# Kernel tuning notes

Measured on AMD Instinct MI355X. Metric: run time of the kernel, lower is better.

## Reference

```python
import jax, jax.numpy as jnp
import numpy as np

D = 1024
H = 16

def setup_inputs() -> dict:
    key = jax.random.key(0)
    k1, k2, k3 = jax.random.split(key, 3)
    x = jax.random.normal(k1, (2, 2048, D), dtype=jnp.float32)
    # torch Linear weights: qkv (3d, d), proj (d, d); y = x @ W.T
    w_qkv = jax.random.normal(k2, (3 * D, D), dtype=jnp.float32) * (1.0 / np.sqrt(D))
    w_proj = jax.random.normal(k3, (D, D), dtype=jnp.float32) * (1.0 / np.sqrt(D))
    return {"x": x, "w_qkv": w_qkv, "w_proj": w_proj}

def reference(x, w_qkv, w_proj):
    B, T, C = x.shape
    hd = C // H  # head dim
    qkv = x @ w_qkv.T                     # [B,T,3C]
    q, k, v = jnp.split(qkv, 3, axis=-1)
    q = q.reshape(B, T, H, hd).transpose(0, 2, 1, 3)  # [B,H,T,hd]
    k = k.reshape(B, T, H, hd).transpose(0, 2, 1, 3)
    v = v.reshape(B, T, H, hd).transpose(0, 2, 1, 3)
    att = jnp.einsum('bhqd,bhkd->bhqk', q, k) * (hd ** -0.5)  # [B,H,T,T]
    mask = jnp.triu(jnp.ones((T, T), dtype=bool), 1)
    att = jnp.where(mask, jnp.float32(-1e9), att)
    att = jax.nn.softmax(att, axis=-1)
    y = jnp.einsum('bhqk,bhkd->bhqd', att, v)  # [B,H,T,hd]
    y = y.transpose(0, 2, 1, 3).reshape(B, T, C)
    return y @ w_proj.T
```

## Files before the change

kernel.cpp:

```cpp
#include <hip/hip_runtime.h>
#include <hip/hip_bf16.h>


typedef __bf16 bf16;
typedef __bf16 bf16x8 __attribute__((ext_vector_type(8)));
typedef float f32x4 __attribute__((ext_vector_type(4)));

__device__ __forceinline__ bf16 f2bf(float f) {
    unsigned u = __builtin_bit_cast(unsigned, f);
    u += 0x7fffu + ((u >> 16) & 1u);
    unsigned short h = (unsigned short)(u >> 16);
    return __builtin_bit_cast(bf16, h);
}
__device__ __forceinline__ bf16 trunc_bf(float f) {
    unsigned u = __builtin_bit_cast(unsigned, f);
    return __builtin_bit_cast(bf16, (unsigned short)(u >> 16));
}

__device__ __forceinline__ bf16x8 ld8f(const float* p) {
    f32x4 a = *(const f32x4*)p;
    f32x4 b = *(const f32x4*)(p + 4);
    bf16x8 r;
#pragma unroll
    for (int i = 0; i < 4; i++) { r[i] = f2bf(a[i]); r[i + 4] = f2bf(b[i]); }
    return r;
}

__device__ __forceinline__ void st_out(bf16* p, float v)  { *p = f2bf(v); }
__device__ __forceinline__ void st_out(float* p, float v) { *p = v; }

__global__ __launch_bounds__(256) void cvt_bf16(const float* __restrict__ src,
                                                bf16* __restrict__ dst, int n) {
    int i = (blockIdx.x * 256 + threadIdx.x) * 8;
    if (i < n) *(bf16x8*)&dst[i] = ld8f(&src[i]);
}

__device__ __forceinline__ void glds16(const bf16* g, bf16* l) {
    __builtin_amdgcn_global_load_lds(
        (const __attribute__((address_space(1))) void*)g,
        (__attribute__((address_space(3))) void*)l, 16, 0, 0);
}

template <typename TC, int BN>
__global__ __launch_bounds__(256) void gemm_glds(const bf16* __restrict__ A, int lda, int aoff,
                                                 const bf16* __restrict__ W,
                                                 TC* __restrict__ C, int N, int K) {
    constexpr int NI = (BN == 128) ? 4 : 2;
    __shared__ bf16 sA[128 * 32];
    __shared__ bf16 sW[BN * 32];
    const int bm = blockIdx.x * 128, bn = blockIdx.y * BN;
    const int tid = threadIdx.x;
    const int wave = tid >> 6, lane = tid & 63;
    const int quad = lane >> 4, l16 = lane & 15;
    const int rbase = (BN == 128) ? (wave >> 1) * 64 : wave * 32;
    const int cbase = (BN == 128) ? (wave & 1) * 64 : 0;
    const int r16 = lane >> 2, cl = lane & 3;
    const int gch = cl ^ ((r16 >> 1) & 3);
    const int sl  = (l16 >> 1) & 3;

    f32x4 acc[NI][4] = {};

    for (int k0 = 0; k0 < K; k0 += 32) {
        __syncthreads();
#pragma unroll
        for (int t = 0; t < 2; t++) {
            int row = wave * 32 + t * 16 + r16;
            glds16(&A[(size_t)(bm + row) * lda + aoff + k0 + gch * 8],
                   &sA[(wave * 32 + t * 16) * 32]);
        }
        if (BN == 128) {
#pragma unroll
            for (int t = 0; t < 2; t++) {
                int row = wave * 32 + t * 16 + r16;
                glds16(&W[(size_t)(bn + row) * K + k0 + gch * 8],
                       &sW[(wave * 32 + t * 16) * 32]);
            }
        } else {
            int row = wave * 16 + r16;
            glds16(&W[(size_t)(bn + row) * K + k0 + gch * 8], &sW[(wave * 16) * 32]);
        }
        __syncthreads();

        bf16x8 af[NI], bfr[4];
#pragma unroll
        for (int i = 0; i < NI; i++)
            af[i] = *(bf16x8*)&sA[(rbase + i * 16 + l16) * 32 + (quad ^ sl) * 8];
#pragma unroll
        for (int j = 0; j < 4; j++)
            bfr[j] = *(bf16x8*)&sW[(cbase + j * 16 + l16) * 32 + (quad ^ sl) * 8];
#pragma unroll
        for (int i = 0; i < NI; i++)
#pragma unroll
            for (int j = 0; j < 4; j++)
                acc[i][j] = __builtin_amdgcn_mfma_f32_16x16x32_bf16(
                    af[i], bfr[j], acc[i][j], 0, 0, 0);
    }

#pragma unroll
    for (int i = 0; i < NI; i++)
#pragma unroll
        for (int j = 0; j < 4; j++)
#pragma unroll
            for (int r = 0; r < 4; r++) {
                int row = bm + rbase + i * 16 + quad * 4 + r;
                int col = bn + cbase + j * 16 + l16;
                st_out(&C[(size_t)row * N + col], acc[i][j][r]);
            }
}

__global__ __launch_bounds__(256) void transpose_v(const bf16* __restrict__ qkv,
                                                   bf16* __restrict__ vt) {
    __shared__ bf16 s[64][72];
    const int tt = blockIdx.x;
    const int bh = blockIdx.y;
    const int b = bh >> 4, h = bh & 15;
    const int tid = threadIdx.x;

    for (int c = tid; c < 512; c += 256) {
        int t = c >> 3, dc = (c & 7) * 8;
        *(bf16x8*)&s[t][dc] =
            *(const bf16x8*)&qkv[((size_t)(b * 2048 + tt * 64 + t)) * 3072 + 2048 + h * 64 + dc];
    }
    __syncthreads();
    for (int c = tid; c < 512; c += 256) {
        int d = c >> 3, tc = (c & 7) * 8;
        bf16x8 o;
#pragma unroll
        for (int e = 0; e < 8; e++) o[e] = s[tc + e][d];
        *(bf16x8*)&vt[((size_t)bh * 64 + d) * 2048 + tt * 64 + tc] = o;
    }
}

__global__ __launch_bounds__(64, 2) void attn(bf16* __restrict__ qkv,
                                              const bf16* __restrict__ vt) {
    const int bh = blockIdx.x;
    const int i  = 63 - blockIdx.y;
    const int b = bh >> 4, h = bh & 15;
    const int lane = threadIdx.x;
    const int quad = lane >> 4, l16 = lane & 15;

    __shared__ bf16 sP[32 * 90];

    bf16* base = qkv + (size_t)b * 2048 * 3072;
    const bf16* vbh = vt + (size_t)bh * 64 * 2048;
    const int qb = i * 32;
    const int kint = i >> 1;
    const float SC = 0.125f * 1.44269504f;

    bf16x8 qa[2][2];
#pragma unroll
    for (int rt = 0; rt < 2; rt++)
#pragma unroll
        for (int c = 0; c < 2; c++)
            qa[rt][c] = *(const bf16x8*)&base[(size_t)(qb + rt * 16 + l16) * 3072 +
                                              h * 64 + c * 32 + quad * 8];

    f32x4 acc[2][4] = {};
    float lpart[2][4] = {};

    auto loadK = [&](int kt, bf16x8 (&kb)[4][2]) {
#pragma unroll
        for (int j = 0; j < 4; j++) {
            const bf16* kr = &base[(size_t)(kt * 64 + j * 16 + l16) * 3072 + 1024 + h * 64];
            kb[j][0] = *(const bf16x8*)&kr[quad * 8];
            kb[j][1] = *(const bf16x8*)&kr[32 + quad * 8];
        }
    };

    auto body = [&](int kt, bool tail, bf16x8 (&kb)[4][2]) {
        bf16x8 vb[4][2];
#pragma unroll
        for (int dt = 0; dt < 4; dt++) {
            const bf16* vr = &vbh[(size_t)(dt * 16 + l16) * 2048 + kt * 64];
            vb[dt][0] = *(const bf16x8*)&vr[quad * 8];
            vb[dt][1] = *(const bf16x8*)&vr[32 + quad * 8];
        }

        f32x4 S[2][4] = {};
#pragma unroll
        for (int j = 0; j < 4; j++)
#pragma unroll
            for (int rt = 0; rt < 2; rt++) {
                S[rt][j] = __builtin_amdgcn_mfma_f32_16x16x32_bf16(qa[rt][0], kb[j][0], S[rt][j], 0, 0, 0);
                S[rt][j] = __builtin_amdgcn_mfma_f32_16x16x32_bf16(qa[rt][1], kb[j][1], S[rt][j], 0, 0, 0);
            }

#pragma unroll
        for (int rt = 0; rt < 2; rt++)
#pragma unroll
            for (int j = 0; j < 4; j++)
#pragma unroll
                for (int r = 0; r < 4; r++) {
                    float p = exp2f(S[rt][j][r] * SC - 8.0f);
                    if (tail) {
                        int kg = kt * 64 + j * 16 + l16;
                        int qg = qb + rt * 16 + quad * 4 + r;
                        p = (kg > qg) ? 0.0f : p;
                    }
                    lpart[rt][r] += p;
                    sP[(rt * 16 + quad * 4 + r) * 90 + j * 16 + l16] = trunc_bf(p);
                }
        __syncthreads();

        bf16x8 pa[2][2];
#pragma unroll
        for (int rt = 0; rt < 2; rt++) {
            pa[rt][0] = *(bf16x8*)&sP[(rt * 16 + l16) * 90 + quad * 8];
            pa[rt][1] = *(bf16x8*)&sP[(rt * 16 + l16) * 90 + 32 + quad * 8];
        }
#pragma unroll
        for (int dt = 0; dt < 4; dt++)
#pragma unroll
            for (int rt = 0; rt < 2; rt++) {
                acc[rt][dt] = __builtin_amdgcn_mfma_f32_16x16x32_bf16(pa[rt][0], vb[dt][0], acc[rt][dt], 0, 0, 0);
                acc[rt][dt] = __builtin_amdgcn_mfma_f32_16x16x32_bf16(pa[rt][1], vb[dt][1], acc[rt][dt], 0, 0, 0);
            }
        __syncthreads();
    };

    bf16x8 kbA[4][2], kbB[4][2];
    loadK(0, kbA);
    int kt = 0;
    while (true) {
        if (kt + 1 <= kint) loadK(kt + 1, kbB);
        body(kt, kt == kint, kbA);
        if (++kt > kint) break;
        if (kt + 1 <= kint) loadK(kt + 1, kbA);
        body(kt, kt == kint, kbB);
        if (++kt > kint) break;
    }

#pragma unroll
    for (int off = 1; off < 16; off <<= 1)
#pragma unroll
        for (int rt = 0; rt < 2; rt++)
#pragma unroll
            for (int r = 0; r < 4; r++)
                lpart[rt][r] += __shfl_xor(lpart[rt][r], off);

#pragma unroll
    for (int rt = 0; rt < 2; rt++)
#pragma unroll
        for (int r = 0; r < 4; r++) {
            float inv = 1.0f / lpart[rt][r];
            int row = qb + rt * 16 + quad * 4 + r;
#pragma unroll
            for (int dt = 0; dt < 4; dt++) {
                int col = h * 64 + dt * 16 + l16;
                base[(size_t)row * 3072 + 2048 + col] = f2bf(acc[rt][dt][r] * inv);
            }
        }
}

extern "C" void kernel_launch(void* const* d_in, const int* in_sizes, int n_in,
                              void* d_out, int out_size, void* d_ws, size_t ws_size,
                              hipStream_t stream) {
    (void)out_size; (void)ws_size;
    const float *x = (const float*)d_in[0], *w_qkv = (const float*)d_in[1],
                *w_proj = (const float*)d_in[2];
    for (int i = 0; i < n_in; i++) {
        if (in_sizes[i] == 4194304) x = (const float*)d_in[i];
        else if (in_sizes[i] == 3145728) w_qkv = (const float*)d_in[i];
        else if (in_sizes[i] == 1048576) w_proj = (const float*)d_in[i];
    }

    float* out = (float*)d_out;
    bf16* xb   = (bf16*)d_out;
    bf16* qkv  = (bf16*)d_ws;
    bf16* r2   = qkv + (size_t)4096 * 3072;
    bf16* wqb  = r2;
    bf16* vt   = r2;
    bf16* wpb  = r2;

    cvt_bf16<<<dim3(2048), dim3(256), 0, stream>>>(x, xb, 4096 * 1024);
    cvt_bf16<<<dim3(1536), dim3(256), 0, stream>>>(w_qkv, wqb, 3072 * 1024);
    gemm_glds<bf16, 128><<<dim3(32, 24), dim3(256), 0, stream>>>(
        xb, 1024, 0, wqb, qkv, 3072, 1024);
    transpose_v<<<dim3(32, 32), dim3(256), 0, stream>>>(qkv, vt);
    attn<<<dim3(32, 64), dim3(64), 0, stream>>>(qkv, vt);
    cvt_bf16<<<dim3(512), dim3(256), 0, stream>>>(w_proj, wpb, 1024 * 1024);
    gemm_glds<float, 128><<<dim3(32, 8), dim3(256), 0, stream>>>(
        qkv, 3072, 2048, wpb, out, 1024, 1024);
}
```

Baseline: 229.5 us.

## Split attention KV loop across four waves with LDS tree reduction

The attention kernel moves from one wave per block to four. Each wave handles every fourth key tile, and the partial accumulators and row sums are combined at the end through a tree reduction in shared memory. The per-tile __syncthreads calls are replaced by per-wave private P buffers and LDS waitcnt fences. The aim is more parallelism per query block on the long causal rows, at the cost of a reduction step and more LDS per block. The reduction works because every wave subtracts the same fixed max (-8.0) before the exponent, so partial sums add directly without rescaling.

```diff
diff --git a/kernel.cpp b/kernel.cpp
--- a/kernel.cpp
+++ b/kernel.cpp
@@ -28,6 +28,10 @@
 
 __device__ __forceinline__ void st_out(bf16* p, float v)  { *p = f2bf(v); }
 __device__ __forceinline__ void st_out(float* p, float v) { *p = v; }
+
+__device__ __forceinline__ void lds_fence() {
+    asm volatile("s_waitcnt lgkmcnt(0)" ::: "memory");
+}
 
 __global__ __launch_bounds__(256) void cvt_bf16(const float* __restrict__ src,
                                                 bf16* __restrict__ dst, int n) {
@@ -131,15 +135,19 @@
     }
 }
 
-__global__ __launch_bounds__(64, 2) void attn(bf16* __restrict__ qkv,
-                                              const bf16* __restrict__ vt) {
+__global__ __launch_bounds__(256, 4) void attn(bf16* __restrict__ qkv,
+                                               const bf16* __restrict__ vt) {
     const int bh = blockIdx.x;
     const int i  = 63 - blockIdx.y;
     const int b = bh >> 4, h = bh & 15;
-    const int lane = threadIdx.x;
+    const int tid  = threadIdx.x;
+    const int wave = tid >> 6;
+    const int lane = tid & 63;
     const int quad = lane >> 4, l16 = lane & 15;
 
-    __shared__ bf16 sP[32 * 90];
+    __shared__ __align__(16) unsigned char smem[23040];
+    bf16*  sPw = (bf16*)smem + wave * 32 * 90;
+    float* sC  = (float*)smem;
 
     bf16* base = qkv + (size_t)b * 2048 * 3072;
     const bf16* vbh = vt + (size_t)bh * 64 * 2048;
@@ -198,15 +206,15 @@
                         p = (kg > qg) ? 0.0f : p;
                     }
                     lpart[rt][r] += p;
-                    sP[(rt * 16 + quad * 4 + r) * 90 + j * 16 + l16] = trunc_bf(p);
+                    sPw[(rt * 16 + quad * 4 + r) * 90 + j * 16 + l16] = trunc_bf(p);
                 }
-        __syncthreads();
+        lds_fence();
 
         bf16x8 pa[2][2];
 #pragma unroll
         for (int rt = 0; rt < 2; rt++) {
-            pa[rt][0] = *(bf16x8*)&sP[(rt * 16 + l16) * 90 + quad * 8];
-            pa[rt][1] = *(bf16x8*)&sP[(rt * 16 + l16) * 90 + 32 + quad * 8];
+            pa[rt][0] = *(bf16x8*)&sPw[(rt * 16 + l16) * 90 + quad * 8];
+            pa[rt][1] = *(bf16x8*)&sPw[(rt * 16 + l16) * 90 + 32 + quad * 8];
         }
 #pragma unroll
         for (int dt = 0; dt < 4; dt++)
@@ -215,20 +223,66 @@
                 acc[rt][dt] = __builtin_amdgcn_mfma_f32_16x16x32_bf16(pa[rt][0], vb[dt][0], acc[rt][dt], 0, 0, 0);
                 acc[rt][dt] = __builtin_amdgcn_mfma_f32_16x16x32_bf16(pa[rt][1], vb[dt][1], acc[rt][dt], 0, 0, 0);
             }
-        __syncthreads();
+        lds_fence();
     };
 
-    bf16x8 kbA[4][2], kbB[4][2];
-    loadK(0, kbA);
-    int kt = 0;
-    while (true) {
-        if (kt + 1 <= kint) loadK(kt + 1, kbB);
-        body(kt, kt == kint, kbA);
-        if (++kt > kint) break;
-        if (kt + 1 <= kint) loadK(kt + 1, kbA);
-        body(kt, kt == kint, kbB);
-        if (++kt > kint) break;
-    }
+    if (wave <= kint) {
+        bf16x8 kbA[4][2], kbB[4][2];
+        int kt = wave;
+        loadK(kt, kbA);
+        while (true) {
+            if (kt + 4 <= kint) loadK(kt + 4, kbB);
+            body(kt, kt == kint, kbA);
+            kt += 4;
+            if (kt > kint) break;
+            if (kt + 4 <= kint) loadK(kt + 4, kbA);
+            body(kt, kt == kint, kbB);
+            kt += 4;
+            if (kt > kint) break;
+        }
+    }
+
+    auto publish = [&](int slot) {
+        float* p = &sC[(size_t)(slot * 64 + lane) * 41];
+#pragma unroll
+        for (int rt = 0; rt < 2; rt++)
+#pragma unroll
+            for (int dt = 0; dt < 4; dt++)
+#pragma unroll
+                for (int r = 0; r < 4; r++)
+                    p[rt * 16 + dt * 4 + r] = acc[rt][dt][r];
+#pragma unroll
+        for (int rt = 0; rt < 2; rt++)
+#pragma unroll
+            for (int r = 0; r < 4; r++)
+                p[32 + rt * 4 + r] = lpart[rt][r];
+    };
+    auto absorb = [&](int slot) {
+        const float* p = &sC[(size_t)(slot * 64 + lane) * 41];
+#pragma unroll
+        for (int rt = 0; rt < 2; rt++)
+#pragma unroll
+            for (int dt = 0; dt < 4; dt++)
+#pragma unroll
+                for (int r = 0; r < 4; r++)
+                    acc[rt][dt][r] += p[rt * 16 + dt * 4 + r];
+#pragma unroll
+        for (int rt = 0; rt < 2; rt++)
+#pragma unroll
+            for (int r = 0; r < 4; r++)
+                lpart[rt][r] += p[32 + rt * 4 + r];
+    };
+
+    __syncthreads();
+    if (wave & 1) publish(wave >> 1);
+    __syncthreads();
+    if (wave == 0) absorb(0);
+    else if (wave == 2) absorb(1);
+    __syncthreads();
+    if (wave == 2) publish(0);
+    __syncthreads();
+    if (wave != 0) return;
+    absorb(0);
 
 #pragma unroll
     for (int off = 1; off < 16; off <<= 1)
@@ -277,7 +331,7 @@
     gemm_glds<bf16, 128><<<dim3(32, 24), dim3(256), 0, stream>>>(
         xb, 1024, 0, wqb, qkv, 3072, 1024);
     transpose_v<<<dim3(32, 32), dim3(256), 0, stream>>>(qkv, vt);
-    attn<<<dim3(32, 64), dim3(64), 0, stream>>>(qkv, vt);
+    attn<<<dim3(32, 64), dim3(256), 0, stream>>>(qkv, vt);
     cvt_bf16<<<dim3(512), dim3(256), 0, stream>>>(w_proj, wpb, 1024 * 1024);
     gemm_glds<float, 128><<<dim3(32, 8), dim3(256), 0, stream>>>(
         qkv, 3072, 2048, wpb, out, 1024, 1024);
```

After: 307.8 us. 1.34x slower.

## Share K/V tiles across four waves via double-buffered LDS staging in attention

Applied to the files above, without the earlier changes.

The attention kernel changes from one 64-thread wave per 32-row query block to 256-thread blocks where four waves handle four consecutive query blocks. Those waves share K and V tiles staged into swizzled, double-buffered LDS with global_load_lds. Each wave now has its own P scratch buffer and uses a waitcnt fence instead of a block barrier. The goal is to cut redundant global K/V reads and overlap loading with compute. The cost is a block-wide barrier per key tile, and waves whose causal range ends early sit idle while the longest wave finishes. Grid ordering is also remapped to interleave heavy and light query groups.

```diff
diff --git a/kernel.cpp b/kernel.cpp
--- a/kernel.cpp
+++ b/kernel.cpp
@@ -28,6 +28,10 @@
 
 __device__ __forceinline__ void st_out(bf16* p, float v)  { *p = f2bf(v); }
 __device__ __forceinline__ void st_out(float* p, float v) { *p = v; }
+
+__device__ __forceinline__ void lds_fence() {
+    asm volatile("s_waitcnt lgkmcnt(0)" ::: "memory");
+}
 
 __global__ __launch_bounds__(256) void cvt_bf16(const float* __restrict__ src,
                                                 bf16* __restrict__ dst, int n) {
@@ -131,21 +135,44 @@
     }
 }
 
-__global__ __launch_bounds__(64, 2) void attn(bf16* __restrict__ qkv,
-                                              const bf16* __restrict__ vt) {
+__global__ __launch_bounds__(256, 2) void attn(bf16* __restrict__ qkv,
+                                               const bf16* __restrict__ vt) {
     const int bh = blockIdx.x;
-    const int i  = 63 - blockIdx.y;
+    const int y  = blockIdx.y;
+    const int g  = (y < 8) ? (15 - y) : (y - 8);
     const int b = bh >> 4, h = bh & 15;
-    const int lane = threadIdx.x;
+    const int tid  = threadIdx.x;
+    const int wave = tid >> 6;
+    const int lane = tid & 63;
     const int quad = lane >> 4, l16 = lane & 15;
 
-    __shared__ bf16 sP[32 * 90];
+    __shared__ bf16 sK[2][64 * 64];
+    __shared__ bf16 sV[2][64 * 64];
+    __shared__ bf16 sP[4][32 * 90];
+    bf16* sPw = sP[wave];
 
     bf16* base = qkv + (size_t)b * 2048 * 3072;
     const bf16* vbh = vt + (size_t)bh * 64 * 2048;
-    const int qb = i * 32;
-    const int kint = i >> 1;
+
+    const int iq = g * 4 + wave;
+    const int qb = iq * 32;
+    const int kint = iq >> 1;
+    const int ktmax = 2 * g + 1;
     const float SC = 0.125f * 1.44269504f;
+
+    const int srow = lane >> 3;
+    const int schk = (lane & 7) ^ srow;
+
+    auto stage = [&](int bufi, int kt) {
+#pragma unroll
+        for (int u = 0; u < 2; u++) {
+            int s = wave * 2 + u;
+            glds16(&base[(size_t)(kt * 64 + s * 8 + srow) * 3072 + 1024 + h * 64 + schk * 8],
+                   &sK[bufi][s * 512]);
+            glds16(&vbh[(size_t)(s * 8 + srow) * 2048 + kt * 64 + schk * 8],
+                   &sV[bufi][s * 512]);
+        }
+    };
 
     bf16x8 qa[2][2];
 #pragma unroll
@@ -157,24 +184,23 @@
 
     f32x4 acc[2][4] = {};
     float lpart[2][4] = {};
-
-    auto loadK = [&](int kt, bf16x8 (&kb)[4][2]) {
-#pragma unroll
-        for (int j = 0; j < 4; j++) {
-            const bf16* kr = &base[(size_t)(kt * 64 + j * 16 + l16) * 3072 + 1024 + h * 64];
-            kb[j][0] = *(const bf16x8*)&kr[quad * 8];
-            kb[j][1] = *(const bf16x8*)&kr[32 + quad * 8];
-        }
-    };
-
-    auto body = [&](int kt, bool tail, bf16x8 (&kb)[4][2]) {
-        bf16x8 vb[4][2];
-#pragma unroll
-        for (int dt = 0; dt < 4; dt++) {
-            const bf16* vr = &vbh[(size_t)(dt * 16 + l16) * 2048 + kt * 64];
-            vb[dt][0] = *(const bf16x8*)&vr[quad * 8];
-            vb[dt][1] = *(const bf16x8*)&vr[32 + quad * 8];
-        }
+    const int sw = l16 & 7;
+
+    auto body = [&](int kt, bool tail, int bufi) {
+        const bf16* K = sK[bufi];
+        const bf16* V = sV[bufi];
+
+        bf16x8 kb[4][2], vb[4][2];
+#pragma unroll
+        for (int j = 0; j < 4; j++)
+#pragma unroll
+            for (int c = 0; c < 2; c++)
+                kb[j][c] = *(const bf16x8*)&K[(j * 16 + l16) * 64 + ((c * 4 + quad) ^ sw) * 8];
+#pragma unroll
+        for (int dt = 0; dt < 4; dt++)
+#pragma unroll
+            for (int c = 0; c < 2; c++)
+                vb[dt][c] = *(const bf16x8*)&V[(dt * 16 + l16) * 64 + ((c * 4 + quad) ^ sw) * 8];
 
         f32x4 S[2][4] = {};
 #pragma unroll
@@ -198,15 +224,15 @@
                         p = (kg > qg) ? 0.0f : p;
                     }
                     lpart[rt][r] += p;
-                    sP[(rt * 16 + quad * 4 + r) * 90 + j * 16 + l16] = trunc_bf(p);
+                    sPw[(rt * 16 + quad * 4 + r) * 90 + j * 16 + l16] = trunc_bf(p);
                 }
-        __syncthreads();
+        lds_fence();
 
         bf16x8 pa[2][2];
 #pragma unroll
         for (int rt = 0; rt < 2; rt++) {
-            pa[rt][0] = *(bf16x8*)&sP[(rt * 16 + l16) * 90 + quad * 8];
-            pa[rt][1] = *(bf16x8*)&sP[(rt * 16 + l16) * 90 + 32 + quad * 8];
+            pa[rt][0] = *(bf16x8*)&sPw[(rt * 16 + l16) * 90 + quad * 8];
+            pa[rt][1] = *(bf16x8*)&sPw[(rt * 16 + l16) * 90 + 32 + quad * 8];
         }
 #pragma unroll
         for (int dt = 0; dt < 4; dt++)
@@ -215,19 +241,19 @@
                 acc[rt][dt] = __builtin_amdgcn_mfma_f32_16x16x32_bf16(pa[rt][0], vb[dt][0], acc[rt][dt], 0, 0, 0);
                 acc[rt][dt] = __builtin_amdgcn_mfma_f32_16x16x32_bf16(pa[rt][1], vb[dt][1], acc[rt][dt], 0, 0, 0);
             }
+        lds_fence();
+    };
+
+    stage(0, 0);
+    asm volatile("s_waitcnt vmcnt(0)" ::: "memory");
+    __syncthreads();
+    int buf = 0;
+    for (int kt = 0; kt <= ktmax; kt++) {
+        if (kt + 1 <= ktmax) stage(buf ^ 1, kt + 1);
+        if (kt <= kint) body(kt, kt == kint, buf);
+        asm volatile("s_waitcnt vmcnt(0)" ::: "memory");
         __syncthreads();
-    };
-
-    bf16x8 kbA[4][2], kbB[4][2];
-    loadK(0, kbA);
-    int kt = 0;
-    while (true) {
-        if (kt + 1 <= kint) loadK(kt + 1, kbB);
-        body(kt, kt == kint, kbA);
-        if (++kt > kint) break;
-        if (kt + 1 <= kint) loadK(kt + 1, kbA);
-        body(kt, kt == kint, kbB);
-        if (++kt > kint) break;
+        buf ^= 1;
     }
 
 #pragma unroll
@@ -277,7 +303,7 @@
     gemm_glds<bf16, 128><<<dim3(32, 24), dim3(256), 0, stream>>>(
         xb, 1024, 0, wqb, qkv, 3072, 1024);
     transpose_v<<<dim3(32, 32), dim3(256), 0, stream>>>(qkv, vt);
-    attn<<<dim3(32, 64), dim3(64), 0, stream>>>(qkv, vt);
+    attn<<<dim3(32, 16), dim3(256), 0, stream>>>(qkv, vt);
     cvt_bf16<<<dim3(512), dim3(256), 0, stream>>>(w_proj, wpb, 1024 * 1024);
     gemm_glds<float, 128><<<dim3(32, 8), dim3(256), 0, stream>>>(
         qkv, 3072, 2048, wpb, out, 1024, 1024);
```

Result: no change. 228.6 us (-0.4%).

## Software-pipeline attention loop: overlap QK of next tile with PV of previous

Applied to the files above, without the earlier changes.

Restructures the attention K-tile loop so that the QK MFMAs for tile kt are issued together with the PV MFMAs for tile kt-1, with a prologue and an epilogue. The P scratch buffer in LDS is doubled so exp writes for the new tile do not clash with reads for the previous one. This lets the per-tile __syncthreads be dropped, which is workable because each block is a single 64-thread wave. MFMA sections are wrapped in s_setprio to raise wave priority. The aim is to hide exp and LDS latency behind matrix work, at the cost of more live registers (two K buffers, V, and S) under the existing launch bounds.

```diff
diff --git a/kernel.cpp b/kernel.cpp
--- a/kernel.cpp
+++ b/kernel.cpp
@@ -139,7 +139,7 @@
     const int lane = threadIdx.x;
     const int quad = lane >> 4, l16 = lane & 15;
 
-    __shared__ bf16 sP[32 * 90];
+    __shared__ bf16 sP[2][32 * 90];
 
     bf16* base = qkv + (size_t)b * 2048 * 3072;
     const bf16* vbh = vt + (size_t)bh * 64 * 2048;
@@ -157,6 +157,7 @@
 
     f32x4 acc[2][4] = {};
     float lpart[2][4] = {};
+    bf16x8 kA[4][2], kB[4][2], vb[4][2];
 
     auto loadK = [&](int kt, bf16x8 (&kb)[4][2]) {
 #pragma unroll
@@ -166,17 +167,16 @@
             kb[j][1] = *(const bf16x8*)&kr[32 + quad * 8];
         }
     };
-
-    auto body = [&](int kt, bool tail, bf16x8 (&kb)[4][2]) {
-        bf16x8 vb[4][2];
+    auto loadV = [&](int kt) {
 #pragma unroll
         for (int dt = 0; dt < 4; dt++) {
             const bf16* vr = &vbh[(size_t)(dt * 16 + l16) * 2048 + kt * 64];
             vb[dt][0] = *(const bf16x8*)&vr[quad * 8];
             vb[dt][1] = *(const bf16x8*)&vr[32 + quad * 8];
         }
-
-        f32x4 S[2][4] = {};
+    };
+    auto qk = [&](f32x4 (&S)[2][4], bf16x8 (&kb)[4][2]) {
+        __builtin_amdgcn_s_setprio(1);
 #pragma unroll
         for (int j = 0; j < 4; j++)
 #pragma unroll
@@ -184,7 +184,27 @@
                 S[rt][j] = __builtin_amdgcn_mfma_f32_16x16x32_bf16(qa[rt][0], kb[j][0], S[rt][j], 0, 0, 0);
                 S[rt][j] = __builtin_amdgcn_mfma_f32_16x16x32_bf16(qa[rt][1], kb[j][1], S[rt][j], 0, 0, 0);
             }
-
+        __builtin_amdgcn_s_setprio(0);
+    };
+    auto pv = [&](int pb) {
+        bf16x8 pa[2][2];
+#pragma unroll
+        for (int rt = 0; rt < 2; rt++) {
+            pa[rt][0] = *(bf16x8*)&sP[pb][(rt * 16 + l16) * 90 + quad * 8];
+            pa[rt][1] = *(bf16x8*)&sP[pb][(rt * 16 + l16) * 90 + 32 + quad * 8];
+        }
+        __builtin_amdgcn_s_setprio(1);
+#pragma unroll
+        for (int dt = 0; dt < 4; dt++)
+#pragma unroll
+            for (int rt = 0; rt < 2; rt++) {
+                acc[rt][dt] = __builtin_amdgcn_mfma_f32_16x16x32_bf16(pa[rt][0], vb[dt][0], acc[rt][dt], 0, 0, 0);
+                acc[rt][dt] = __builtin_amdgcn_mfma_f32_16x16x32_bf16(pa[rt][1], vb[dt][1], acc[rt][dt], 0, 0, 0);
+            }
+        __builtin_amdgcn_s_setprio(0);
+    };
+    auto expwr = [&](f32x4 (&S)[2][4], int kt, bool tail) {
+        bf16* sPw = sP[kt & 1];
 #pragma unroll
         for (int rt = 0; rt < 2; rt++)
 #pragma unroll
@@ -198,37 +218,42 @@
                         p = (kg > qg) ? 0.0f : p;
                     }
                     lpart[rt][r] += p;
-                    sP[(rt * 16 + quad * 4 + r) * 90 + j * 16 + l16] = trunc_bf(p);
+                    sPw[(rt * 16 + quad * 4 + r) * 90 + j * 16 + l16] = trunc_bf(p);
                 }
-        __syncthreads();
-
-        bf16x8 pa[2][2];
-#pragma unroll
-        for (int rt = 0; rt < 2; rt++) {
-            pa[rt][0] = *(bf16x8*)&sP[(rt * 16 + l16) * 90 + quad * 8];
-            pa[rt][1] = *(bf16x8*)&sP[(rt * 16 + l16) * 90 + 32 + quad * 8];
-        }
-#pragma unroll
-        for (int dt = 0; dt < 4; dt++)
-#pragma unroll
-            for (int rt = 0; rt < 2; rt++) {
-                acc[rt][dt] = __builtin_amdgcn_mfma_f32_16x16x32_bf16(pa[rt][0], vb[dt][0], acc[rt][dt], 0, 0, 0);
-                acc[rt][dt] = __builtin_amdgcn_mfma_f32_16x16x32_bf16(pa[rt][1], vb[dt][1], acc[rt][dt], 0, 0, 0);
-            }
-        __syncthreads();
-    };
-
-    bf16x8 kbA[4][2], kbB[4][2];
-    loadK(0, kbA);
-    int kt = 0;
-    while (true) {
-        if (kt + 1 <= kint) loadK(kt + 1, kbB);
-        body(kt, kt == kint, kbA);
+    };
+
+    loadK(0, kA);
+    if (kint >= 1) loadK(1, kB);
+    {
+        f32x4 S[2][4] = {};
+        qk(S, kA);
+        expwr(S, 0, kint == 0);
+    }
+
+    int kt = 1;
+    while (kt <= kint) {
+        {
+            loadV(kt - 1);
+            if (kt + 1 <= kint) loadK(kt + 1, kA);
+            f32x4 S[2][4] = {};
+            qk(S, kB);
+            pv((kt - 1) & 1);
+            expwr(S, kt, kt == kint);
+        }
         if (++kt > kint) break;
-        if (kt + 1 <= kint) loadK(kt + 1, kbA);
-        body(kt, kt == kint, kbB);
-        if (++kt > kint) break;
-    }
+        {
+            loadV(kt - 1);
+            if (kt + 1 <= kint) loadK(kt + 1, kB);
+            f32x4 S[2][4] = {};
+            qk(S, kA);
+            pv((kt - 1) & 1);
+            expwr(S, kt, kt == kint);
+        }
+        ++kt;
+    }
+
+    loadV(kint);
+    pv(kint & 1);
 
 #pragma unroll
     for (int off = 1; off < 16; off <<= 1)
```

Measured after the change: 231.5 us. No clear change (+0.9%).
